# Performance work log

Measured on AMD Instinct MI355X. Metric: run time of the kernel, lower is better.

## Reference

```python
import jax, jax.numpy as jnp
import numpy as np

L, H, C, V, B, T, Q = 6, 8, 512, 32000, 2, 4096, 256
N = C // H
LN_EPS = 1e-5
GN_EPS = 1e-5 * 64  # matches nn.GroupNorm(n_head, C, eps=1e-05*64)


def _shift(x):
    # ZeroPad2d((0,0,1,-1)): x[t] -> x[t-1], zero at t=0
    return jnp.concatenate([jnp.zeros_like(x[:, :1]), x[:, :-1]], axis=1)


def _layernorm(x, w):
    mu = x.mean(-1, keepdims=True)
    var = jnp.var(x, axis=-1, keepdims=True)
    return (x - mu) * jax.lax.rsqrt(var + LN_EPS) * w


def _time_mix(x, maa_k, maa_v, maa_r, maa_g, tdecay, tfaaaa, Wr, Wk, Wv, Wg, Wo, gn_w, gn_b):
    Bsz, Tlen, Cd = x.shape
    xx = _shift(x) - x
    xk = x + xx * maa_k
    xv = x + xx * maa_v
    xr = x + xx * maa_r
    xg = x + xx * maa_g
    r = (xr @ Wr.T).reshape(Bsz, Tlen, H, N).transpose(0, 2, 1, 3)   # B H T N
    k = (xk @ Wk.T).reshape(Bsz, Tlen, H, N).transpose(0, 2, 3, 1)   # B H N T
    v = (xv @ Wv.T).reshape(Bsz, Tlen, H, N).transpose(0, 2, 1, 3)   # B H T N
    g = jax.nn.silu(xg @ Wg.T)
    wdec = jnp.exp(-jnp.exp(tdecay))            # [H], per-head decay in (0,1)
    u = tfaaaa                                  # [H], 'first token' bonus
    ws = (wdec ** Q)[None, :, None, None]       # state decay across a chunk
    jj = jnp.arange(Q)
    wkv = (wdec[:, None] ** (Q - 1 - jj))[None, :, None, :]  # [1,H,1,Q]
    wb = (wdec[:, None] ** jj)[None, :, :, None]              # [1,H,Q,1]
    d = jj[:, None] - jj[None, :]                              # i - j
    # intra-chunk decay matrix: W[i,j] = u (i==j), wdec^(i-j-1) (i>j), 0 (i<j)
    Wmat = jnp.where(d > 0, wdec[:, None, None] ** jnp.maximum(d - 1, 0), 0.0)
    Wmat = (Wmat + u[:, None, None] * jnp.eye(Q, dtype=x.dtype))[None]  # [1,H,Q,Q]
    nc = Tlen // Q
    rc = r.reshape(Bsz, H, nc, Q, N).transpose(2, 0, 1, 3, 4)  # [nc,B,H,Q,N]
    kc = k.reshape(Bsz, H, N, nc, Q).transpose(3, 0, 1, 2, 4)  # [nc,B,H,N,Q]
    vc = v.reshape(Bsz, H, nc, Q, N).transpose(2, 0, 1, 3, 4)  # [nc,B,H,Q,N]

    def step(state, inp):
        rr, kk, vv = inp
        y = ((rr @ kk) * Wmat) @ vv + (rr @ state) * wb
        new_state = ws * state + (kk * wkv) @ vv
        return new_state, y

    state0 = jnp.zeros((Bsz, H, N, N), dtype=x.dtype)
    _, yc = jax.lax.scan(step, state0, (rc, kc, vc))
    y = yc.transpose(1, 2, 0, 3, 4).reshape(Bsz, H, Tlen, N).transpose(0, 2, 1, 3)  # B T H N
    # GroupNorm(n_head groups) == per (b,t,h) normalization over head dim N
    mu = y.mean(-1, keepdims=True)
    var = jnp.var(y, axis=-1, keepdims=True)
    y = (y - mu) * jax.lax.rsqrt(var + GN_EPS)
    y = y.reshape(Bsz, Tlen, Cd) * gn_w + gn_b
    return (y * g) @ Wo.T


def _channel_mix(x, cmaa_k, cmaa_r, Wck, Wcv, Wcr):
    xx = _shift(x) - x
    xk = x + xx * cmaa_k
    xr = x + xx * cmaa_r
    h = jnp.square(jax.nn.relu(xk @ Wck.T))
    h = h @ Wcv.T
    return jax.nn.sigmoid(xr @ Wcr.T) * h


def _forward(idx, wte, wpe, ln1_w, ln2_w, lnf_w, maa_k, maa_v, maa_r, maa_g, tdecay, tfaaaa,
             Wr, Wk, Wv, Wg, Wo, gn_w, gn_b, cmaa_k, cmaa_r, Wck, Wcv, Wcr):
    t = idx.shape[1]
    x = wte[idx] + wpe[:t]
    for l in range(L):
        x = x + _time_mix(_layernorm(x, ln1_w[l]), maa_k[l], maa_v[l], maa_r[l], maa_g[l],
                          tdecay[l], tfaaaa[l], Wr[l], Wk[l], Wv[l], Wg[l], Wo[l], gn_w[l], gn_b[l])
        x = x + _channel_mix(_layernorm(x, ln2_w[l]), cmaa_k[l], cmaa_r[l], Wck[l], Wcv[l], Wcr[l])
    x = _layernorm(x, lnf_w)
    logits = x[:, -1:, :] @ wte.T  # targets=None path: only last position
    return logits


def setup_inputs() -> dict:
    key = jax.random.key(0)
    ks = jax.random.split(key, 12)
    idx = jax.random.randint(ks[0], (B, T), 0, V)
    # structured per-layer init tensors (exact formulas from __init__)
    ddd = np.arange(C, dtype=np.float32) / C
    hh = np.arange(H, dtype=np.float32) / (H - 1)
    maa_k = np.zeros((L, C), np.float32); maa_v = np.zeros((L, C), np.float32)
    maa_r = np.zeros((L, C), np.float32); maa_g = np.zeros((L, C), np.float32)
    tdecay = np.zeros((L, H), np.float32); tfaaaa = np.zeros((L, H), np.float32)
    cmaa_k = np.zeros((L, C), np.float32); cmaa_r = np.zeros((L, C), np.float32)
    for l in range(L):
        r0 = l / max(L - 1, 1)
        r1 = 1.0 - l / L
        maa_k[l] = 1.0 - ddd ** r1
        maa_v[l] = 1.0 - (ddd ** r1 + 0.3 * r0)
        maa_r[l] = 1.0 - ddd ** (0.5 * r1)
        maa_g[l] = 1.0 - ddd ** (0.5 * r1)
        tdecay[l] = -6.0 + 5.0 * hh ** (0.7 + 1.3 * r0)
        tfaaaa[l] = r0 * (1.0 - hh)
        cmaa_k[l] = 1.0 - ddd ** r1
        cmaa_r[l] = 1.0 - ddd ** r1
    s = 0.02
    return {
        'idx': idx,
        'wte': jax.random.normal(ks[1], (V, C), jnp.float32) * s,
        'wpe': jax.random.normal(ks[2], (T, C), jnp.float32) * s,
        'ln1_w': jnp.ones((L, C), jnp.float32),
        'ln2_w': jnp.ones((L, C), jnp.float32),
        'lnf_w': jnp.ones((C,), jnp.float32),
        'maa_k': jnp.asarray(maa_k), 'maa_v': jnp.asarray(maa_v),
        'maa_r': jnp.asarray(maa_r), 'maa_g': jnp.asarray(maa_g),
        'tdecay': jnp.asarray(tdecay), 'tfaaaa': jnp.asarray(tfaaaa),
        'Wr': jax.random.normal(ks[3], (L, C, C), jnp.float32) * s,
        'Wk': jax.random.normal(ks[4], (L, C, C), jnp.float32) * s,
        'Wv': jax.random.normal(ks[5], (L, C, C), jnp.float32) * s,
        'Wg': jax.random.normal(ks[6], (L, C, C), jnp.float32) * s,
        'Wo': jax.random.normal(ks[7], (L, C, C), jnp.float32) * (s / np.sqrt(2 * L)),
        'gn_w': jnp.ones((L, C), jnp.float32),
        'gn_b': jnp.zeros((L, C), jnp.float32),
        'cmaa_k': jnp.asarray(cmaa_k), 'cmaa_r': jnp.asarray(cmaa_r),
        'Wck': jax.random.normal(ks[8], (L, 3 * C, C), jnp.float32) * s,
        'Wcv': jax.random.normal(ks[9], (L, C, 3 * C), jnp.float32) * s,
        'Wcr': jax.random.normal(ks[10], (L, C, C), jnp.float32) * s,
    }


def reference(idx, wte, wpe, ln1_w, ln2_w, lnf_w, maa_k, maa_v, maa_r, maa_g, tdecay, tfaaaa,
              Wr, Wk, Wv, Wg, Wo, gn_w, gn_b, cmaa_k, cmaa_r, Wck, Wcv, Wcr):
    return _forward(idx, wte, wpe, ln1_w, ln2_w, lnf_w, maa_k, maa_v, maa_r, maa_g, tdecay,
                    tfaaaa, Wr, Wk, Wv, Wg, Wo, gn_w, gn_b, cmaa_k, cmaa_r, Wck, Wcv, Wcr)
```

## Files before the change

### kernel.cpp

```cpp
#include <hip/hip_runtime.h>

#define L_ 6
#define H_ 8
#define C_ 512
#define V_ 32000
#define B_ 2
#define T_ 4096
#define Q_ 256
#define N_ 64
#define NC_ 16
#define M_ 8192

typedef unsigned short u16;
typedef __attribute__((ext_vector_type(8))) short bf16x8;
typedef __attribute__((ext_vector_type(4))) float f32x4;

__device__ __forceinline__ float bf2f(u16 u){
  return __uint_as_float(((unsigned int)u) << 16);
}
__device__ __forceinline__ u16 f2bf(float f){
  unsigned int x = __float_as_uint(f);
  return (u16)((x + 0x7fffu + ((x >> 16) & 1u)) >> 16);
}

__device__ __forceinline__ void gl_lds16(const u16* g, u16* l){
  __builtin_amdgcn_global_load_lds((const __attribute__((address_space(1))) void*)g,
                                   (__attribute__((address_space(3))) void*)l, 16, 0, 0);
}

__global__ __launch_bounds__(256) void detect_kernel(const void* __restrict__ probe,
                                                     int* __restrict__ flag){
  __shared__ int cnt;
  if (threadIdx.x == 0) cnt = 0;
  __syncthreads();
  const u16* p = (const u16*)probe;
  int c = 0;
  for (int i = threadIdx.x; i < 2048; i += 256){
    int e = (p[i] >> 7) & 0xFF;
    if (e >= 128) c++;
  }
  atomicAdd(&cnt, c);
  __syncthreads();
  if (threadIdx.x == 0) *flag = (cnt > 32) ? 1 : 0;
}

struct CvtTab { const void* s[23]; int off8[24]; int bstart[24]; };

__global__ __launch_bounds__(256) void convert_all(CvtTab t, u16* __restrict__ pool,
                                                   const int* __restrict__ flag){
  int i = 0;
  #pragma unroll
  for (int k = 1; k < 23; k++) if ((int)blockIdx.x >= t.bstart[k]) i = k;
  const void* sp = t.s[0];
  #pragma unroll
  for (int k = 1; k < 23; k++) if (i == k) sp = t.s[k];
  const int n8 = t.off8[i+1] - t.off8[i];
  const int nb = t.bstart[i+1] - t.bstart[i];
  const int lb = (int)blockIdx.x - t.bstart[i];
  uint4* dp = (uint4*)pool + t.off8[i];
  const int stride = nb * 256;
  int j = lb*256 + (int)threadIdx.x;
  if (*flag){
    const float4* sf = (const float4*)sp;
    for (; j + stride < n8; j += 2*stride){
      float4 a0 = sf[2*j], a1 = sf[2*j+1];
      int j2 = j + stride;
      float4 b0 = sf[2*j2], b1 = sf[2*j2+1];
      uint4 r0, r1;
      r0.x = (unsigned)f2bf(a0.x) | ((unsigned)f2bf(a0.y) << 16);
      r0.y = (unsigned)f2bf(a0.z) | ((unsigned)f2bf(a0.w) << 16);
      r0.z = (unsigned)f2bf(a1.x) | ((unsigned)f2bf(a1.y) << 16);
      r0.w = (unsigned)f2bf(a1.z) | ((unsigned)f2bf(a1.w) << 16);
      r1.x = (unsigned)f2bf(b0.x) | ((unsigned)f2bf(b0.y) << 16);
      r1.y = (unsigned)f2bf(b0.z) | ((unsigned)f2bf(b0.w) << 16);
      r1.z = (unsigned)f2bf(b1.x) | ((unsigned)f2bf(b1.y) << 16);
      r1.w = (unsigned)f2bf(b1.z) | ((unsigned)f2bf(b1.w) << 16);
      dp[j] = r0; dp[j2] = r1;
    }
    for (; j < n8; j += stride){
      float4 a0 = sf[2*j], a1 = sf[2*j+1];
      uint4 r0;
      r0.x = (unsigned)f2bf(a0.x) | ((unsigned)f2bf(a0.y) << 16);
      r0.y = (unsigned)f2bf(a0.z) | ((unsigned)f2bf(a0.w) << 16);
      r0.z = (unsigned)f2bf(a1.x) | ((unsigned)f2bf(a1.y) << 16);
      r0.w = (unsigned)f2bf(a1.z) | ((unsigned)f2bf(a1.w) << 16);
      dp[j] = r0;
    }
  } else {
    const uint4* s4 = (const uint4*)sp;
    for (; j + 3*stride < n8; j += 4*stride){
      uint4 a = s4[j], b = s4[j+stride], c = s4[j+2*stride], d = s4[j+3*stride];
      dp[j] = a; dp[j+stride] = b; dp[j+2*stride] = c; dp[j+3*stride] = d;
    }
    for (; j < n8; j += stride) dp[j] = s4[j];
  }
}

__global__ __launch_bounds__(256) void embed_kernel(const int* __restrict__ idx,
    const u16* __restrict__ wte, const u16* __restrict__ wpe, float* __restrict__ x){
  int row = blockIdx.x;
  int t = row & (T_-1);
  int tok = idx[row];
  const u16* we = wte + (size_t)tok * C_;
  const u16* wp = wpe + (size_t)t * C_;
  float* xo = x + (size_t)row * C_;
  int c = threadIdx.x;
  xo[c]     = bf2f(we[c])     + bf2f(wp[c]);
  xo[c+256] = bf2f(we[c+256]) + bf2f(wp[c+256]);
}

__global__ __launch_bounds__(256) void ln_tmix_kernel(const float* __restrict__ x,
    const u16* __restrict__ w,
    const u16* __restrict__ mk, const u16* __restrict__ mv,
    const u16* __restrict__ mr, const u16* __restrict__ mg,
    u16* __restrict__ xk, u16* __restrict__ xv, u16* __restrict__ xr, u16* __restrict__ xg){
  int row = blockIdx.x; int t = row & (T_-1);
  size_t off = (size_t)row*C_;
  const float* cur = x + off;
  int c = threadIdx.x;
  float v0 = cur[c], v1 = cur[c+256];
  float p0 = 0.f, p1 = 0.f;
  if (t){ p0 = cur[c - C_]; p1 = cur[c+256 - C_]; }
  float s = v0+v1, ss = v0*v0+v1*v1;
  float sp = p0+p1, ssp = p0*p0+p1*p1;
  int lane = c & 63, wid = c >> 6;
  #pragma unroll
  for (int o=32;o>0;o>>=1){
    s  += __shfl_down(s,o,64);  ss  += __shfl_down(ss,o,64);
    sp += __shfl_down(sp,o,64); ssp += __shfl_down(ssp,o,64);
  }
  __shared__ float r1[4], r2[4], r3[4], r4[4];
  if (lane==0){ r1[wid]=s; r2[wid]=ss; r3[wid]=sp; r4[wid]=ssp; }
  __syncthreads();
  if (c==0){
    float a =r1[0]+r1[1]+r1[2]+r1[3], bq=r2[0]+r2[1]+r2[2]+r2[3];
    float ap=r3[0]+r3[1]+r3[2]+r3[3], bp=r4[0]+r4[1]+r4[2]+r4[3];
    float mu  = a *(1.f/C_); float var  = bq*(1.f/C_) - mu*mu;
    float mup = ap*(1.f/C_); float varp = bp*(1.f/C_) - mup*mup;
    r1[0]=mu;  r2[0]=rsqrtf(fmaxf(var ,0.f)+1e-5f);
    r3[0]=mup; r4[0]=rsqrtf(fmaxf(varp,0.f)+1e-5f);
  }
  __syncthreads();
  float mu=r1[0], inv=r2[0], mup=r3[0], invp=r4[0];
  #pragma unroll
  for (int p=0;p<2;p++){
    int cc = c + p*256;
    float wc = bf2f(w[cc]);
    float xc = ((p?v1:v0)-mu)*inv*wc;
    float xp = t ? ((p?p1:p0)-mup)*invp*wc : 0.f;
    float xx = xp - xc;
    xk[off+cc] = f2bf(xc + xx*bf2f(mk[cc]));
    xv[off+cc] = f2bf(xc + xx*bf2f(mv[cc]));
    xr[off+cc] = f2bf(xc + xx*bf2f(mr[cc]));
    xg[off+cc] = f2bf(xc + xx*bf2f(mg[cc]));
  }
}

__global__ __launch_bounds__(256) void ln_cmix_kernel(const float* __restrict__ x,
    const u16* __restrict__ w,
    const u16* __restrict__ mk, const u16* __restrict__ mr,
    u16* __restrict__ xk, u16* __restrict__ xr){
  int row = blockIdx.x; int t = row & (T_-1);
  size_t off = (size_t)row*C_;
  const float* cur = x + off;
  int c = threadIdx.x;
  float v0 = cur[c], v1 = cur[c+256];
  float p0 = 0.f, p1 = 0.f;
  if (t){ p0 = cur[c - C_]; p1 = cur[c+256 - C_]; }
  float s = v0+v1, ss = v0*v0+v1*v1;
  float sp = p0+p1, ssp = p0*p0+p1*p1;
  int lane = c & 63, wid = c >> 6;
  #pragma unroll
  for (int o=32;o>0;o>>=1){
    s  += __shfl_down(s,o,64);  ss  += __shfl_down(ss,o,64);
    sp += __shfl_down(sp,o,64); ssp += __shfl_down(ssp,o,64);
  }
  __shared__ float r1[4], r2[4], r3[4], r4[4];
  if (lane==0){ r1[wid]=s; r2[wid]=ss; r3[wid]=sp; r4[wid]=ssp; }
  __syncthreads();
  if (c==0){
    float a =r1[0]+r1[1]+r1[2]+r1[3], bq=r2[0]+r2[1]+r2[2]+r2[3];
    float ap=r3[0]+r3[1]+r3[2]+r3[3], bp=r4[0]+r4[1]+r4[2]+r4[3];
    float mu  = a *(1.f/C_); float var  = bq*(1.f/C_) - mu*mu;
    float mup = ap*(1.f/C_); float varp = bp*(1.f/C_) - mup*mup;
    r1[0]=mu;  r2[0]=rsqrtf(fmaxf(var ,0.f)+1e-5f);
    r3[0]=mup; r4[0]=rsqrtf(fmaxf(varp,0.f)+1e-5f);
  }
  __syncthreads();
  float mu=r1[0], inv=r2[0], mup=r3[0], invp=r4[0];
  #pragma unroll
  for (int p=0;p<2;p++){
    int cc = c + p*256;
    float wc = bf2f(w[cc]);
    float xc = ((p?v1:v0)-mu)*inv*wc;
    float xp = t ? ((p?p1:p0)-mup)*invp*wc : 0.f;
    float xx = xp - xc;
    xk[off+cc] = f2bf(xc + xx*bf2f(mk[cc]));
    xr[off+cc] = f2bf(xc + xx*bf2f(mr[cc]));
  }
}

__global__ __launch_bounds__(256) void lnf_last(const float* __restrict__ x,
    const u16* __restrict__ w, float* __restrict__ xf){
  int b = blockIdx.x;
  const float* xr = x + ((size_t)b*T_ + (T_-1))*C_;
  int c = threadIdx.x;
  float v0 = xr[c], v1 = xr[c+256];
  float s = v0+v1, ss = v0*v0+v1*v1;
  int lane = c & 63, wid = c >> 6;
  #pragma unroll
  for (int o=32;o>0;o>>=1){ s += __shfl_down(s,o,64); ss += __shfl_down(ss,o,64); }
  __shared__ float r1[4], r2[4];
  if (lane==0){ r1[wid]=s; r2[wid]=ss; }
  __syncthreads();
  if (c==0){
    float a=r1[0]+r1[1]+r1[2]+r1[3], bq=r2[0]+r2[1]+r2[2]+r2[3];
    float mu = a*(1.f/C_);
    float var = bq*(1.f/C_) - mu*mu;
    r1[0]=mu; r2[0]=rsqrtf(fmaxf(var,0.f)+1e-5f);
  }
  __syncthreads();
  float mu=r1[0], inv=r2[0];
  xf[b*C_+c]     = (v0-mu)*inv*bf2f(w[c]);
  xf[b*C_+c+256] = (v1-mu)*inv*bf2f(w[c+256]);
}

#define ACT_F32 0
#define ACT_RELU2_BF16 1
#define ACT_ADD_F32 2
#define ACT_BF16 3
#define ACT_CMIX 4
#define ACT_KT 5
#define ACT_VT 6
#define ACT_SIG_BF16 7

template<int ACT>
__device__ __forceinline__ void gemm_mfma_body(const u16* __restrict__ X, const u16* __restrict__ W,
    float* __restrict__ Yf, u16* __restrict__ Yb, const u16* __restrict__ AuxB,
    u16* __restrict__ Yt, const u16* __restrict__ td,
    int Ndim, int Kdim, int bm, int bn){
  __shared__ __align__(16) u16 SH[128*64 + 64*64];
  u16* Al = SH;
  u16* Bl = SH + 128*64;
  const int tid = threadIdx.x;
  const int wv = tid >> 6, ln = tid & 63;
  const int m16 = ln & 15, q = ln >> 4;

  f32x4 acc[2][4];
  #pragma unroll
  for (int i=0;i<2;i++)
    #pragma unroll
    for (int j=0;j<4;j++) acc[i][j] = f32x4{0.f,0.f,0.f,0.f};

  const int r0 = wv*8 + (ln >> 3);
  const int c0 = (ln & 7)*8;
  const u16* ga = X + (size_t)(bm + r0)*Kdim + c0;
  const u16* gb = W + (size_t)(bn + r0)*Kdim + c0;
  u16* la = Al + r0*64 + c0;
  u16* lb = Bl + r0*64 + c0;

  for (int k0=0; k0<Kdim; k0+=64){
    #pragma unroll
    for (int s=0;s<4;s++)
      gl_lds16(ga + (size_t)(s*32)*Kdim + k0, la + s*2048);
    #pragma unroll
    for (int s=0;s<2;s++)
      gl_lds16(gb + (size_t)(s*32)*Kdim + k0, lb + s*2048);
    __syncthreads();
    #pragma unroll
    for (int kh=0; kh<2; kh++){
      bf16x8 af[2], bfr[4];
      #pragma unroll
      for (int i=0;i<2;i++) af[i]  = *(const bf16x8*)(Al + (wv*32 + i*16 + m16)*64 + kh*32 + q*8);
      #pragma unroll
      for (int j=0;j<4;j++) bfr[j] = *(const bf16x8*)(Bl + (j*16 + m16)*64 + kh*32 + q*8);
      #pragma unroll
      for (int i=0;i<2;i++)
        #pragma unroll
        for (int j=0;j<4;j++)
          acc[i][j] = __builtin_amdgcn_mfma_f32_16x16x32_bf16(af[i], bfr[j], acc[i][j], 0, 0, 0);
    }
    __syncthreads();
  }

  if (ACT==ACT_KT || ACT==ACT_VT){
    u16* TT = SH;
    const float wdec_s = (ACT==ACT_KT) ? expf(-expf(bf2f(td[(bn>>6)&7]))) : 0.f;
    const int tchunk0 = bm & (Q_-1);
    #pragma unroll
    for (int i=0;i<2;i++){
      const int tloc = wv*32 + i*16 + q*4;
      #pragma unroll
      for (int j=0;j<4;j++){
        const int n = j*16 + m16;
        union { ushort4 v; u16 e[4]; } pk;
        #pragma unroll
        for (int r=0;r<4;r++){
          float v = acc[i][j][r];
          if (ACT==ACT_KT){
            Yb[(size_t)(bm + tloc + r)*Ndim + (bn + n)] = f2bf(v);
            pk.e[r] = f2bf(v * powf(wdec_s, (float)(Q_-1 - (tchunk0 + tloc + r))));
          } else {
            pk.e[r] = f2bf(v);
          }
        }
        *(ushort4*)&TT[n*136 + tloc] = pk.v;
      }
    }
    __syncthreads();
    const int bb = bm >> 12, tt0 = bm & (T_-1);
    const int hh = (bn >> 6) & 7;
    const int nn2 = wv*16 + (ln>>2), seg = ln & 3;
    const u16* srcp = TT + nn2*136 + seg*32;
    u16* dstp = Yt + ((size_t)(((bb<<3)+hh)*64 + nn2))*T_ + tt0 + seg*32;
    #pragma unroll
    for (int k2=0;k2<4;k2++)
      *(uint4*)(dstp + k2*8) = *(const uint4*)(srcp + k2*8);
    return;
  }
  #pragma unroll
  for (int i=0;i<2;i++){
    int row = bm + wv*32 + i*16 + q*4;
    #pragma unroll
    for (int j=0;j<4;j++){
      int col = bn + j*16 + m16;
      #pragma unroll
      for (int r=0;r<4;r++){
        size_t off = (size_t)(row + r)*Ndim + col;
        float v = acc[i][j][r];
        if (ACT==ACT_F32) Yf[off] = v;
        else if (ACT==ACT_RELU2_BF16){ float rr = v>0.f ? v : 0.f; Yb[off] = f2bf(rr*rr); }
        else if (ACT==ACT_BF16) Yb[off] = f2bf(v);
        else if (ACT==ACT_SIG_BF16) Yb[off] = f2bf(1.f/(1.f+expf(-v)));
        else if (ACT==ACT_CMIX){ Yf[off] += v * bf2f(AuxB[off]); }
        else Yf[off] += v;
      }
    }
  }
}

template<int ACT>
__global__ __launch_bounds__(256,4) void gemm_mfma(const u16* __restrict__ X, const u16* __restrict__ W,
    float* __restrict__ Yf, u16* __restrict__ Yb, int Ndim, int Kdim){
  gemm_mfma_body<ACT>(X, W, Yf, Yb, nullptr, nullptr, nullptr, Ndim, Kdim,
                      blockIdx.x*128, blockIdx.y*64);
}

__global__ __launch_bounds__(256,4) void gemm4_mfma(const u16* __restrict__ Abase,
    const u16* __restrict__ W0, const u16* __restrict__ W1,
    const u16* __restrict__ W2, const u16* __restrict__ W3,
    u16* __restrict__ Rb, u16* __restrict__ Kb, u16* __restrict__ Kt,
    u16* __restrict__ Vt, u16* __restrict__ Gb, const u16* __restrict__ td){
  const size_t MC = (size_t)M_*C_;
  const int bm = blockIdx.x*128, bn = blockIdx.y*64;
  switch (blockIdx.z){
    case 0:  gemm_mfma_body<ACT_BF16>(Abase + 2*MC, W0, nullptr, Rb, nullptr, nullptr, nullptr,
                                      C_, C_, bm, bn); break;
    case 1:  gemm_mfma_body<ACT_KT>(Abase, W1, nullptr, Kb, nullptr, Kt, td,
                                    C_, C_, bm, bn); break;
    case 2:  gemm_mfma_body<ACT_VT>(Abase + 1*MC, W2, nullptr, nullptr, nullptr, Vt, nullptr,
                                    C_, C_, bm, bn); break;
    default: gemm_mfma_body<ACT_BF16>(Abase + 3*MC, W3, nullptr, Gb, nullptr, nullptr, nullptr,
                                      C_, C_, bm, bn); break;
  }
}

__global__ __launch_bounds__(256,4) void gemm_ck_cr(const u16* __restrict__ MK, const u16* __restrict__ Wck,
    u16* __restrict__ H1, const u16* __restrict__ MV, const u16* __restrict__ Wcr,
    u16* __restrict__ RRb){
  if (blockIdx.y < 24)
    gemm_mfma_body<ACT_RELU2_BF16>(MK, Wck, nullptr, H1, nullptr, nullptr, nullptr, 3*C_, C_,
                                   blockIdx.x*128, blockIdx.y*64);
  else
    gemm_mfma_body<ACT_SIG_BF16>(MV, Wcr, nullptr, RRb, nullptr, nullptr, nullptr, C_, C_,
                                 blockIdx.x*128, (blockIdx.y-24)*64);
}

__global__ __launch_bounds__(256,4) void gemm_cmix(const u16* __restrict__ H1, const u16* __restrict__ Wcv,
    float* __restrict__ X, const u16* __restrict__ RRb){
  gemm_mfma_body<ACT_CMIX>(H1, Wcv, X, nullptr, RRb, nullptr, nullptr, C_, 3*C_,
                           blockIdx.x*128, blockIdx.y*64);
}

__global__ __launch_bounds__(256) void wkv_state_mfma(const u16* __restrict__ Kt,
    const u16* __restrict__ Vt, float* __restrict__ S){
  const int c = blockIdx.x, bh = blockIdx.y;
  const int tid = threadIdx.x, wv = tid >> 6, ln = tid & 63;
  const int m16 = ln & 15, q = ln >> 4;
  const u16* ka = Kt + (size_t)(bh*N_ + wv*16 + m16)*T_ + c*Q_;
  const u16* vb = Vt + (size_t)(bh*N_ + m16)*T_ + c*Q_;
  f32x4 acc[4];
  #pragma unroll
  for (int nt=0;nt<4;++nt) acc[nt] = f32x4{0.f,0.f,0.f,0.f};
  #pragma unroll
  for (int ks=0; ks<8; ++ks){
    bf16x8 af = *(const bf16x8*)(ka + ks*32 + q*8);
    #pragma unroll
    for (int nt=0;nt<4;++nt){
      bf16x8 bv = *(const bf16x8*)(vb + (size_t)(nt*16)*T_ + ks*32 + q*8);
      acc[nt] = __builtin_amdgcn_mfma_f32_16x16x32_bf16(af, bv, acc[nt], 0,0,0);
    }
  }
  float* Sp = S + ((size_t)bh*NC_ + c)*(N_*N_);
  #pragma unroll
  for (int nt=0;nt<4;++nt)
    #pragma unroll
    for (int r=0;r<4;++r)
      Sp[(wv*16 + q*4 + r)*N_ + nt*16 + m16] = acc[nt][r];
}

__global__ __launch_bounds__(256) void wkv_prefix(float* __restrict__ S, const u16* __restrict__ td){
  const int bh = blockIdx.x, h = bh&7;
  const float wdec = expf(-expf(bf2f(td[h])));
  const float wsd = powf(wdec, (float)Q_);
  float* Sp = S + (size_t)bh*NC_*N_*N_;
  for (int e=threadIdx.x; e<N_*N_; e+=256){
    float cur = 0.f;
    for (int cc=0;cc<NC_;++cc){
      float sc = Sp[(size_t)cc*N_*N_ + e];
      Sp[(size_t)cc*N_*N_ + e] = cur;
      cur = wsd*cur + sc;
    }
  }
}

__global__ __launch_bounds__(256) void wkv_fused(const u16* __restrict__ Rb,
    const u16* __restrict__ Kb, const u16* __restrict__ Vt, const float* __restrict__ S,
    const u16* __restrict__ td, const u16* __restrict__ tf,
    const u16* __restrict__ gnw, const u16* __restrict__ gnb, const u16* __restrict__ g,
    u16* __restrict__ out){
  __shared__ float wpow[Q_];
  __shared__ float st[64][68];
  __shared__ float rs[64][68];
  __shared__ __align__(16) float ylds[64][68];
  u16 (*P)[16][72] = reinterpret_cast<u16(*)[16][72]>(&ylds[0][0]);
  const int c = blockIdx.x>>2, ip = blockIdx.x&3;
  const int bh = blockIdx.y, b = bh>>3, h = bh&7;
  const int tid = threadIdx.x, wv = tid >> 6, ln = tid & 63;
  const int m16 = ln & 15, q = ln >> 4;
  const int tx = tid&15, ty = tid>>4;
  const float wdec = expf(-expf(bf2f(td[h])));
  const float uu = bf2f(tf[h]);
  wpow[tid] = powf(wdec, (float)tid);
  const float* Sp = S + ((size_t)bh*NC_ + c)*(N_*N_);
  for (int e=tid;e<N_*N_;e+=256) st[e>>6][e&63] = Sp[e];
  const size_t base = ((size_t)b*T_ + (size_t)c*Q_)*C_ + h*N_;
  const int i0 = ip*64;
  {
    const int rrr = tid >> 6, cc2 = tid & 63;
    for (int it=0;it<16;++it){ int i=it*4+rrr; rs[i][cc2]=bf2f(Rb[base+(size_t)(i0+i)*C_+cc2]); }
  }
  __syncthreads();
  const int iw0 = ip*64 + wv*16;
  const u16* rrow = Rb + base + (size_t)(iw0 + m16)*C_;
  bf16x8 af0 = *(const bf16x8*)(rrow + q*8);
  bf16x8 af1 = *(const bf16x8*)(rrow + 32 + q*8);
  f32x4 acc[4];
  #pragma unroll
  for (int nt=0;nt<4;++nt) acc[nt] = f32x4{0.f,0.f,0.f,0.f};
  const int irow = iw0 + q*4;
  const u16* vtb = Vt + (size_t)(bh*N_)*T_ + (size_t)c*Q_;
  for (int jt=0; jt<=ip; ++jt){
    f32x4 s[4];
    #pragma unroll
    for (int j2=0;j2<4;++j2) s[j2] = f32x4{0.f,0.f,0.f,0.f};
    #pragma unroll
    for (int j2=0;j2<4;++j2){
      const u16* kr = Kb + base + (size_t)(jt*64 + j2*16 + m16)*C_;
      bf16x8 b0 = *(const bf16x8*)(kr + q*8);
      bf16x8 b1 = *(const bf16x8*)(kr + 32 + q*8);
      s[j2] = __builtin_amdgcn_mfma_f32_16x16x32_bf16(af0, b0, s[j2], 0,0,0);
      s[j2] = __builtin_amdgcn_mfma_f32_16x16x32_bf16(af1, b1, s[j2], 0,0,0);
    }
    #pragma unroll
    for (int j2=0;j2<4;++j2){
      int jc = jt*64 + j2*16 + m16;
      #pragma unroll
      for (int r=0;r<4;++r){
        int ic = irow + r;
        float w = (jc < ic) ? wpow[ic-jc-1] : ((jc==ic) ? uu : 0.f);
        P[wv][q*4+r][j2*16+m16] = f2bf(s[j2][r]*w);
      }
    }
    __asm__ volatile("s_waitcnt lgkmcnt(0)" ::: "memory");
    #pragma unroll
    for (int kp=0;kp<2;++kp){
      bf16x8 ap = *(const bf16x8*)&P[wv][m16][kp*32 + q*8];
      #pragma unroll
      for (int nt=0;nt<4;++nt){
        bf16x8 bv = *(const bf16x8*)(vtb + (size_t)(nt*16 + m16)*T_ + jt*64 + kp*32 + q*8);
        acc[nt] = __builtin_amdgcn_mfma_f32_16x16x32_bf16(ap, bv, acc[nt], 0,0,0);
      }
    }
  }
  __syncthreads();
  #pragma unroll
  for (int nt=0;nt<4;++nt)
    #pragma unroll
    for (int r=0;r<4;++r)
      ylds[wv*16 + q*4 + r][nt*16 + m16] = acc[nt][r];
  __syncthreads();
  float acc2[4][4] = {};
  #pragma unroll
  for (int kk4=0;kk4<16;++kk4){
    f32x4 sv[4], rv[4];
    #pragma unroll
    for (int kkk=0;kkk<4;++kkk) sv[kkk] = *(const f32x4*)&st[kk4*4+kkk][tx*4];
    #pragma unroll
    for (int ii=0;ii<4;++ii)    rv[ii]  = *(const f32x4*)&rs[ty*4+ii][kk4*4];
    #pragma unroll
    for (int ii=0;ii<4;++ii)
      #pragma unroll
      for (int kkk=0;kkk<4;++kkk)
        #pragma unroll
        for (int nn=0;nn<4;++nn)
          acc2[ii][nn] += rv[ii][kkk]*sv[kkk][nn];
  }
  #pragma unroll
  for (int ii=0;ii<4;ii++){
    int tl = ty*4+ii;
    int il = i0 + tl;
    size_t roff = base + (size_t)il*C_;
    float w = wpow[il];
    f32x4 yv = *(const f32x4*)&ylds[tl][tx*4];
    float val[4];
    float s=0.f, ss=0.f;
    #pragma unroll
    for (int nn=0;nn<4;nn++){
      float v = yv[nn] + w*acc2[ii][nn];
      val[nn]=v; s+=v; ss+=v*v;
    }
    #pragma unroll
    for (int o=8;o>0;o>>=1){ s+=__shfl_xor(s,o,64); ss+=__shfl_xor(ss,o,64); }
    float mu = s*(1.f/N_);
    float var = ss*(1.f/N_) - mu*mu;
    float inv = rsqrtf(fmaxf(var,0.f) + 6.4e-4f);
    union { ushort4 v; u16 e[4]; } gv, ov;
    gv.v = *(const ushort4*)(g + roff + tx*4);
    #pragma unroll
    for (int nn=0;nn<4;nn++){
      int ci = h*N_ + tx*4 + nn;
      float gg = bf2f(gv.e[nn]);
      float sil = gg/(1.f+expf(-gg));
      ov.e[nn] = f2bf(((val[nn]-mu)*inv*bf2f(gnw[ci]) + bf2f(gnb[ci]))*sil);
    }
    *(ushort4*)(out + roff + tx*4) = ov.v;
  }
}

__global__ __launch_bounds__(256) void logits_kernel(const float* __restrict__ xf,
    const u16* __restrict__ wte, void* __restrict__ out, const int* __restrict__ flag){
  const int wid = threadIdx.x>>6, lane = threadIdx.x&63;
  const int gw = blockIdx.x*4 + wid;
  const int b = gw / V_, v = gw - b*V_;
  const u16* wrow = wte + (size_t)v*C_;
  const float* xr = xf + b*C_;
  union {uint4 q; u16 h[8];} uu;
  uu.q = *(const uint4*)(wrow + lane*8);
  float s = 0.f;
  #pragma unroll
  for (int j=0;j<8;j++) s += bf2f(uu.h[j])*xr[lane*8+j];
  #pragma unroll
  for (int o=32;o>0;o>>=1) s += __shfl_down(s,o,64);
  if (lane==0){
    size_t o = (size_t)b*V_ + v;
    if (*flag) ((float*)out)[o] = s;
    else       ((u16*)out)[o]   = f2bf(s);
  }
}

extern "C" void kernel_launch(void* const* d_in, const int* in_sizes, int n_in,
                              void* d_out, int out_size, void* d_ws, size_t ws_size,
                              hipStream_t stream){
  (void)out_size; (void)ws_size; (void)n_in;
  const int* idx  = (const int*)d_in[0];

  char* ws = (char*)d_ws;
  const size_t MC  = (size_t)M_*C_;
  size_t o = 0;
  int* flag = (int*)(ws + o);            o += 1024;
  float* X   = (float*)(ws + o);         o += MC*4;
  u16* MK = (u16*)(ws + o);              o += MC*2;
  u16* MV = (u16*)(ws + o);              o += MC*2;
  u16* MR = (u16*)(ws + o);              o += MC*2;
  u16* MG = (u16*)(ws + o);              o += MC*2;
  u16* Rb = (u16*)(ws + o);              o += MC*2;
  u16* Kb = (u16*)(ws + o);              o += MC*2;
  u16* Kt = (u16*)(ws + o);              o += MC*2;
  u16* Gb = (u16*)(ws + o);              o += MC*2;
  u16* Vt = (u16*)(ws + o);              o += MC*2;
  float* XF = (float*)(ws + o);          o += 65536;
  u16* pool = (u16*)(ws + o);
  u16* YGN = MK;
  float* S  = (float*)MR;
  u16* H1 = Rb;
  u16* RRb = MR;

  detect_kernel<<<1,256,0,stream>>>(d_in[12], flag);
  u16* cw[24];
  CvtTab tab;
  int nblocks;
  {
    size_t poff = 0; int acc8 = 0, bacc = 0;
    long long total8 = 0;
    for (int i=1;i<24;i++) total8 += (long long)(in_sizes[i] >> 3);
    for (int i=1;i<24;i++){
      cw[i] = pool + poff; poff += (size_t)in_sizes[i];
      tab.s[i-1] = d_in[i];
      tab.off8[i-1] = acc8;
      tab.bstart[i-1] = bacc;
      int n8 = in_sizes[i] >> 3;
      int nb = (int)(((long long)n8 * 2048 + total8 - 1) / total8);
      if (nb < 1) nb = 1;
      acc8 += n8; bacc += nb;
    }
    tab.off8[23] = acc8; tab.bstart[23] = bacc;
    nblocks = bacc;
  }
  convert_all<<<nblocks,256,0,stream>>>(tab, pool, flag);
  const u16* wte  = cw[1];  const u16* wpe  = cw[2];
  const u16* ln1w = cw[3];  const u16* ln2w = cw[4];  const u16* lnfw = cw[5];
  const u16* maak = cw[6];  const u16* maav = cw[7];
  const u16* maar = cw[8];  const u16* maag = cw[9];
  const u16* tdec = cw[10]; const u16* tfir = cw[11];
  const u16* Wr   = cw[12]; const u16* Wk   = cw[13]; const u16* Wv   = cw[14];
  const u16* Wg   = cw[15]; const u16* Wo   = cw[16];
  const u16* gnw  = cw[17]; const u16* gnb  = cw[18];
  const u16* cmk  = cw[19]; const u16* cmr  = cw[20];
  const u16* Wck  = cw[21]; const u16* Wcv  = cw[22]; const u16* Wcr  = cw[23];

  embed_kernel<<<M_,256,0,stream>>>(idx,wte,wpe,X);
  dim3 gsq(M_/128, C_/64);
  dim3 g4 (M_/128, C_/64, 4);
  dim3 gckcr(M_/128, 32);
  for (int l=0;l<L_;++l){
    ln_tmix_kernel<<<M_,256,0,stream>>>(X, ln1w+l*C_, maak+l*C_, maav+l*C_, maar+l*C_,
                                        maag+l*C_, MK,MV,MR,MG);
    gemm4_mfma<<<g4,256,0,stream>>>(MK, Wr+(size_t)l*C_*C_, Wk+(size_t)l*C_*C_,
                                    Wv+(size_t)l*C_*C_, Wg+(size_t)l*C_*C_,
                                    Rb, Kb, Kt, Vt, Gb, tdec+l*H_);
    wkv_state_mfma<<<dim3(NC_, B_*H_),256,0,stream>>>(Kt, Vt, S);
    wkv_prefix<<<B_*H_,256,0,stream>>>(S, tdec+l*H_);
    wkv_fused<<<dim3(NC_*4, B_*H_),256,0,stream>>>(Rb, Kb, Vt, S, tdec+l*H_, tfir+l*H_,
                                                   gnw+l*C_, gnb+l*C_, Gb, YGN);
    gemm_mfma<ACT_ADD_F32><<<gsq,256,0,stream>>>(YGN, Wo+(size_t)l*C_*C_, X, nullptr, C_, C_);
    ln_cmix_kernel<<<M_,256,0,stream>>>(X, ln2w+l*C_, cmk+l*C_, cmr+l*C_, MK, MV);
    gemm_ck_cr<<<gckcr,256,0,stream>>>(MK, Wck+(size_t)l*3*C_*C_, H1,
                                       MV, Wcr+(size_t)l*C_*C_, RRb);
    gemm_cmix<<<gsq,256,0,stream>>>(H1, Wcv+(size_t)l*3*C_*C_, X, RRb);
  }
  lnf_last<<<B_,256,0,stream>>>(X, lnfw, XF);
  logits_kernel<<<(B_*V_)/4,256,0,stream>>>(XF, wte, d_out, flag);
}
```

Before: 1.673 ms.

## Skip bf16 weight copy via pointer table, widen GEMM tiles, split K/V transpose

Adds a device pointer table filled at runtime, so when inputs are already bf16 the kernels read the raw input buffers instead of copying every weight into a pool. The conversion kernel now returns early in that case. The QKVG and channel-mix GEMMs move to 128x128 tiles, and the fused transpose/decay epilogue is pulled out into a separate kvtrans kernel using swizzled LDS. powf is replaced by exp2f. Larger tiles raise register and LDS pressure, and the separate transpose adds an extra pass over K and V.

```diff
diff --git a/kernel.cpp b/kernel.cpp
--- a/kernel.cpp
+++ b/kernel.cpp
@@ -44,10 +44,20 @@
   if (threadIdx.x == 0) *flag = (cnt > 32) ? 1 : 0;
 }
 
+struct PtrTab { const void* raw[23]; long long off[23]; };
+
+__global__ __launch_bounds__(64) void fill_ptab(PtrTab pt, const u16* __restrict__ pool,
+    const int* __restrict__ flag, const u16** __restrict__ ptab){
+  int i = threadIdx.x;
+  if (i < 23)
+    ptab[i+1] = (*flag) ? (pool + pt.off[i]) : (const u16*)pt.raw[i];
+}
+
 struct CvtTab { const void* s[23]; int off8[24]; int bstart[24]; };
 
 __global__ __launch_bounds__(256) void convert_all(CvtTab t, u16* __restrict__ pool,
                                                    const int* __restrict__ flag){
+  if (!*flag) return;
   int i = 0;
   #pragma unroll
   for (int k = 1; k < 23; k++) if ((int)blockIdx.x >= t.bstart[k]) i = k;
@@ -59,45 +69,22 @@
   const int lb = (int)blockIdx.x - t.bstart[i];
   uint4* dp = (uint4*)pool + t.off8[i];
   const int stride = nb * 256;
-  int j = lb*256 + (int)threadIdx.x;
-  if (*flag){
-    const float4* sf = (const float4*)sp;
-    for (; j + stride < n8; j += 2*stride){
-      float4 a0 = sf[2*j], a1 = sf[2*j+1];
-      int j2 = j + stride;
-      float4 b0 = sf[2*j2], b1 = sf[2*j2+1];
-      uint4 r0, r1;
-      r0.x = (unsigned)f2bf(a0.x) | ((unsigned)f2bf(a0.y) << 16);
-      r0.y = (unsigned)f2bf(a0.z) | ((unsigned)f2bf(a0.w) << 16);
-      r0.z = (unsigned)f2bf(a1.x) | ((unsigned)f2bf(a1.y) << 16);
-      r0.w = (unsigned)f2bf(a1.z) | ((unsigned)f2bf(a1.w) << 16);
-      r1.x = (unsigned)f2bf(b0.x) | ((unsigned)f2bf(b0.y) << 16);
-      r1.y = (unsigned)f2bf(b0.z) | ((unsigned)f2bf(b0.w) << 16);
-      r1.z = (unsigned)f2bf(b1.x) | ((unsigned)f2bf(b1.y) << 16);
-      r1.w = (unsigned)f2bf(b1.z) | ((unsigned)f2bf(b1.w) << 16);
-      dp[j] = r0; dp[j2] = r1;
-    }
-    for (; j < n8; j += stride){
-      float4 a0 = sf[2*j], a1 = sf[2*j+1];
-      uint4 r0;
-      r0.x = (unsigned)f2bf(a0.x) | ((unsigned)f2bf(a0.y) << 16);
-      r0.y = (unsigned)f2bf(a0.z) | ((unsigned)f2bf(a0.w) << 16);
-      r0.z = (unsigned)f2bf(a1.x) | ((unsigned)f2bf(a1.y) << 16);
-      r0.w = (unsigned)f2bf(a1.z) | ((unsigned)f2bf(a1.w) << 16);
-      dp[j] = r0;
-    }
-  } else {
-    const uint4* s4 = (const uint4*)sp;
-    for (; j + 3*stride < n8; j += 4*stride){
-      uint4 a = s4[j], b = s4[j+stride], c = s4[j+2*stride], d = s4[j+3*stride];
-      dp[j] = a; dp[j+stride] = b; dp[j+2*stride] = c; dp[j+3*stride] = d;
-    }
-    for (; j < n8; j += stride) dp[j] = s4[j];
+  const float4* sf = (const float4*)sp;
+  for (int j = lb*256 + (int)threadIdx.x; j < n8; j += stride){
+    float4 a0 = sf[2*j], a1 = sf[2*j+1];
+    uint4 r0;
+    r0.x = (unsigned)f2bf(a0.x) | ((unsigned)f2bf(a0.y) << 16);
+    r0.y = (unsigned)f2bf(a0.z) | ((unsigned)f2bf(a0.w) << 16);
+    r0.z = (unsigned)f2bf(a1.x) | ((unsigned)f2bf(a1.y) << 16);
+    r0.w = (unsigned)f2bf(a1.z) | ((unsigned)f2bf(a1.w) << 16);
+    dp[j] = r0;
   }
 }
 
 __global__ __launch_bounds__(256) void embed_kernel(const int* __restrict__ idx,
-    const u16* __restrict__ wte, const u16* __restrict__ wpe, float* __restrict__ x){
+    const u16* const* __restrict__ ptab, float* __restrict__ x){
+  const u16* wte = ptab[1];
+  const u16* wpe = ptab[2];
   int row = blockIdx.x;
   int t = row & (T_-1);
   int tok = idx[row];
@@ -110,10 +97,13 @@
 }
 
 __global__ __launch_bounds__(256) void ln_tmix_kernel(const float* __restrict__ x,
-    const u16* __restrict__ w,
-    const u16* __restrict__ mk, const u16* __restrict__ mv,
-    const u16* __restrict__ mr, const u16* __restrict__ mg,
+    const u16* const* __restrict__ ptab, int l,
     u16* __restrict__ xk, u16* __restrict__ xv, u16* __restrict__ xr, u16* __restrict__ xg){
+  const u16* w  = ptab[3] + l*C_;
+  const u16* mk = ptab[6] + l*C_;
+  const u16* mv = ptab[7] + l*C_;
+  const u16* mr = ptab[8] + l*C_;
+  const u16* mg = ptab[9] + l*C_;
   int row = blockIdx.x; int t = row & (T_-1);
   size_t off = (size_t)row*C_;
   const float* cur = x + off;
@@ -157,9 +147,11 @@
 }
 
 __global__ __launch_bounds__(256) void ln_cmix_kernel(const float* __restrict__ x,
-    const u16* __restrict__ w,
-    const u16* __restrict__ mk, const u16* __restrict__ mr,
+    const u16* const* __restrict__ ptab, int l,
     u16* __restrict__ xk, u16* __restrict__ xr){
+  const u16* w  = ptab[4]  + l*C_;
+  const u16* mk = ptab[19] + l*C_;
+  const u16* mr = ptab[20] + l*C_;
   int row = blockIdx.x; int t = row & (T_-1);
   size_t off = (size_t)row*C_;
   const float* cur = x + off;
@@ -201,7 +193,8 @@
 }
 
 __global__ __launch_bounds__(256) void lnf_last(const float* __restrict__ x,
-    const u16* __restrict__ w, float* __restrict__ xf){
+    const u16* const* __restrict__ ptab, float* __restrict__ xf){
+  const u16* w = ptab[5];
   int b = blockIdx.x;
   const float* xr = x + ((size_t)b*T_ + (T_-1))*C_;
   int c = threadIdx.x;
@@ -225,23 +218,18 @@
   xf[b*C_+c+256] = (v1-mu)*inv*bf2f(w[c+256]);
 }
 
-#define ACT_F32 0
 #define ACT_RELU2_BF16 1
 #define ACT_ADD_F32 2
 #define ACT_BF16 3
 #define ACT_CMIX 4
-#define ACT_KT 5
-#define ACT_VT 6
 #define ACT_SIG_BF16 7
 
 template<int ACT>
 __device__ __forceinline__ void gemm_mfma_body(const u16* __restrict__ X, const u16* __restrict__ W,
     float* __restrict__ Yf, u16* __restrict__ Yb, const u16* __restrict__ AuxB,
-    u16* __restrict__ Yt, const u16* __restrict__ td,
     int Ndim, int Kdim, int bm, int bn){
-  __shared__ __align__(16) u16 SH[128*64 + 64*64];
-  u16* Al = SH;
-  u16* Bl = SH + 128*64;
+  __shared__ __align__(16) u16 Al[128*64];
+  __shared__ __align__(16) u16 Bl[64*64];
   const int tid = threadIdx.x;
   const int wv = tid >> 6, ln = tid & 63;
   const int m16 = ln & 15, q = ln >> 4;
@@ -283,41 +271,6 @@
     __syncthreads();
   }
 
-  if (ACT==ACT_KT || ACT==ACT_VT){
-    u16* TT = SH;
-    const float wdec_s = (ACT==ACT_KT) ? expf(-expf(bf2f(td[(bn>>6)&7]))) : 0.f;
-    const int tchunk0 = bm & (Q_-1);
-    #pragma unroll
-    for (int i=0;i<2;i++){
-      const int tloc = wv*32 + i*16 + q*4;
-      #pragma unroll
-      for (int j=0;j<4;j++){
-        const int n = j*16 + m16;
-        union { ushort4 v; u16 e[4]; } pk;
-        #pragma unroll
-        for (int r=0;r<4;r++){
-          float v = acc[i][j][r];
-          if (ACT==ACT_KT){
-            Yb[(size_t)(bm + tloc + r)*Ndim + (bn + n)] = f2bf(v);
-            pk.e[r] = f2bf(v * powf(wdec_s, (float)(Q_-1 - (tchunk0 + tloc + r))));
-          } else {
-            pk.e[r] = f2bf(v);
-          }
-        }
-        *(ushort4*)&TT[n*136 + tloc] = pk.v;
-      }
-    }
-    __syncthreads();
-    const int bb = bm >> 12, tt0 = bm & (T_-1);
-    const int hh = (bn >> 6) & 7;
-    const int nn2 = wv*16 + (ln>>2), seg = ln & 3;
-    const u16* srcp = TT + nn2*136 + seg*32;
-    u16* dstp = Yt + ((size_t)(((bb<<3)+hh)*64 + nn2))*T_ + tt0 + seg*32;
-    #pragma unroll
-    for (int k2=0;k2<4;k2++)
-      *(uint4*)(dstp + k2*8) = *(const uint4*)(srcp + k2*8);
-    return;
-  }
   #pragma unroll
   for (int i=0;i<2;i++){
     int row = bm + wv*32 + i*16 + q*4;
@@ -328,58 +281,153 @@
       for (int r=0;r<4;r++){
         size_t off = (size_t)(row + r)*Ndim + col;
         float v = acc[i][j][r];
-        if (ACT==ACT_F32) Yf[off] = v;
+        if (ACT==ACT_ADD_F32) Yf[off] += v;
+        else if (ACT==ACT_CMIX){ Yf[off] += v * bf2f(AuxB[off]); }
+        else if (ACT==ACT_BF16) Yb[off] = f2bf(v);
+      }
+    }
+  }
+}
+
+template<int ACT>
+__device__ __forceinline__ void gemm128_body(const u16* __restrict__ X, const u16* __restrict__ W,
+    u16* __restrict__ Yb, int Ndim, int Kdim, int bm, int bn){
+  __shared__ __align__(16) u16 Al[128*64];
+  __shared__ __align__(16) u16 Bl[128*64];
+  const int tid = threadIdx.x;
+  const int wv = tid >> 6, ln = tid & 63;
+  const int m16 = ln & 15, q = ln >> 4;
+
+  f32x4 acc[2][8];
+  #pragma unroll
+  for (int i=0;i<2;i++)
+    #pragma unroll
+    for (int j=0;j<8;j++) acc[i][j] = f32x4{0.f,0.f,0.f,0.f};
+
+  const int r0 = wv*8 + (ln >> 3);
+  const int c0 = (ln & 7)*8;
+  const u16* ga = X + (size_t)(bm + r0)*Kdim + c0;
+  const u16* gb = W + (size_t)(bn + r0)*Kdim + c0;
+  u16* la = Al + r0*64 + c0;
+  u16* lb = Bl + r0*64 + c0;
+
+  for (int k0=0; k0<Kdim; k0+=64){
+    #pragma unroll
+    for (int s=0;s<4;s++)
+      gl_lds16(ga + (size_t)(s*32)*Kdim + k0, la + s*2048);
+    #pragma unroll
+    for (int s=0;s<4;s++)
+      gl_lds16(gb + (size_t)(s*32)*Kdim + k0, lb + s*2048);
+    __syncthreads();
+    #pragma unroll
+    for (int kh=0; kh<2; kh++){
+      bf16x8 af0 = *(const bf16x8*)(Al + (wv*32 + m16)*64      + kh*32 + q*8);
+      bf16x8 af1 = *(const bf16x8*)(Al + (wv*32 + 16 + m16)*64 + kh*32 + q*8);
+      #pragma unroll
+      for (int j=0;j<8;j++){
+        bf16x8 bfr = *(const bf16x8*)(Bl + (j*16 + m16)*64 + kh*32 + q*8);
+        acc[0][j] = __builtin_amdgcn_mfma_f32_16x16x32_bf16(af0, bfr, acc[0][j], 0, 0, 0);
+        acc[1][j] = __builtin_amdgcn_mfma_f32_16x16x32_bf16(af1, bfr, acc[1][j], 0, 0, 0);
+      }
+    }
+    __syncthreads();
+  }
+
+  #pragma unroll
+  for (int i=0;i<2;i++){
+    int row = bm + wv*32 + i*16 + q*4;
+    #pragma unroll
+    for (int j=0;j<8;j++){
+      int col = bn + j*16 + m16;
+      #pragma unroll
+      for (int r=0;r<4;r++){
+        size_t off = (size_t)(row + r)*Ndim + col;
+        float v = acc[i][j][r];
+        if (ACT==ACT_BF16) Yb[off] = f2bf(v);
         else if (ACT==ACT_RELU2_BF16){ float rr = v>0.f ? v : 0.f; Yb[off] = f2bf(rr*rr); }
-        else if (ACT==ACT_BF16) Yb[off] = f2bf(v);
         else if (ACT==ACT_SIG_BF16) Yb[off] = f2bf(1.f/(1.f+expf(-v)));
-        else if (ACT==ACT_CMIX){ Yf[off] += v * bf2f(AuxB[off]); }
-        else Yf[off] += v;
       }
     }
   }
 }
 
-template<int ACT>
-__global__ __launch_bounds__(256,4) void gemm_mfma(const u16* __restrict__ X, const u16* __restrict__ W,
-    float* __restrict__ Yf, u16* __restrict__ Yb, int Ndim, int Kdim){
-  gemm_mfma_body<ACT>(X, W, Yf, Yb, nullptr, nullptr, nullptr, Ndim, Kdim,
-                      blockIdx.x*128, blockIdx.y*64);
-}
-
-__global__ __launch_bounds__(256,4) void gemm4_mfma(const u16* __restrict__ Abase,
-    const u16* __restrict__ W0, const u16* __restrict__ W1,
-    const u16* __restrict__ W2, const u16* __restrict__ W3,
-    u16* __restrict__ Rb, u16* __restrict__ Kb, u16* __restrict__ Kt,
-    u16* __restrict__ Vt, u16* __restrict__ Gb, const u16* __restrict__ td){
+__global__ __launch_bounds__(256,3) void gemm4_mfma(const u16* const* __restrict__ ptab, int l,
+    const u16* __restrict__ Abase,
+    u16* __restrict__ Rb, u16* __restrict__ Kb, u16* __restrict__ Vb, u16* __restrict__ Gb){
   const size_t MC = (size_t)M_*C_;
-  const int bm = blockIdx.x*128, bn = blockIdx.y*64;
+  const size_t ws = (size_t)l*C_*C_;
+  const int bm = blockIdx.x*128, bn = blockIdx.y*128;
   switch (blockIdx.z){
-    case 0:  gemm_mfma_body<ACT_BF16>(Abase + 2*MC, W0, nullptr, Rb, nullptr, nullptr, nullptr,
-                                      C_, C_, bm, bn); break;
-    case 1:  gemm_mfma_body<ACT_KT>(Abase, W1, nullptr, Kb, nullptr, Kt, td,
-                                    C_, C_, bm, bn); break;
-    case 2:  gemm_mfma_body<ACT_VT>(Abase + 1*MC, W2, nullptr, nullptr, nullptr, Vt, nullptr,
-                                    C_, C_, bm, bn); break;
-    default: gemm_mfma_body<ACT_BF16>(Abase + 3*MC, W3, nullptr, Gb, nullptr, nullptr, nullptr,
-                                      C_, C_, bm, bn); break;
-  }
-}
-
-__global__ __launch_bounds__(256,4) void gemm_ck_cr(const u16* __restrict__ MK, const u16* __restrict__ Wck,
-    u16* __restrict__ H1, const u16* __restrict__ MV, const u16* __restrict__ Wcr,
-    u16* __restrict__ RRb){
-  if (blockIdx.y < 24)
-    gemm_mfma_body<ACT_RELU2_BF16>(MK, Wck, nullptr, H1, nullptr, nullptr, nullptr, 3*C_, C_,
-                                   blockIdx.x*128, blockIdx.y*64);
+    case 0:  gemm128_body<ACT_BF16>(Abase + 2*MC, ptab[12]+ws, Rb, C_, C_, bm, bn); break;
+    case 1:  gemm128_body<ACT_BF16>(Abase,        ptab[13]+ws, Kb, C_, C_, bm, bn); break;
+    case 2:  gemm128_body<ACT_BF16>(Abase + 1*MC, ptab[14]+ws, Vb, C_, C_, bm, bn); break;
+    default: gemm128_body<ACT_BF16>(Abase + 3*MC, ptab[15]+ws, Gb, C_, C_, bm, bn); break;
+  }
+}
+
+__global__ __launch_bounds__(256,3) void gemm_ck_cr(const u16* const* __restrict__ ptab, int l,
+    const u16* __restrict__ MK, u16* __restrict__ H1,
+    const u16* __restrict__ MV, u16* __restrict__ RRb){
+  if (blockIdx.y < 12)
+    gemm128_body<ACT_RELU2_BF16>(MK, ptab[21]+(size_t)l*3*C_*C_, H1, 3*C_, C_,
+                                 blockIdx.x*128, blockIdx.y*128);
   else
-    gemm_mfma_body<ACT_SIG_BF16>(MV, Wcr, nullptr, RRb, nullptr, nullptr, nullptr, C_, C_,
-                                 blockIdx.x*128, (blockIdx.y-24)*64);
-}
-
-__global__ __launch_bounds__(256,4) void gemm_cmix(const u16* __restrict__ H1, const u16* __restrict__ Wcv,
-    float* __restrict__ X, const u16* __restrict__ RRb){
-  gemm_mfma_body<ACT_CMIX>(H1, Wcv, X, nullptr, RRb, nullptr, nullptr, C_, 3*C_,
-                           blockIdx.x*128, blockIdx.y*64);
+    gemm128_body<ACT_SIG_BF16>(MV, ptab[23]+(size_t)l*C_*C_, RRb, C_, C_,
+                               blockIdx.x*128, (blockIdx.y-12)*128);
+}
+
+__global__ __launch_bounds__(256,4) void gemm_wo(const u16* const* __restrict__ ptab, int l,
+    const u16* __restrict__ YGN, float* __restrict__ X){
+  gemm_mfma_body<ACT_ADD_F32>(YGN, ptab[16]+(size_t)l*C_*C_, X, nullptr, nullptr,
+                              C_, C_, blockIdx.x*128, blockIdx.y*64);
+}
+
+__global__ __launch_bounds__(256,4) void gemm_cmix(const u16* const* __restrict__ ptab, int l,
+    const u16* __restrict__ H1, float* __restrict__ X, const u16* __restrict__ RRb){
+  gemm_mfma_body<ACT_CMIX>(H1, ptab[22]+(size_t)l*3*C_*C_, X, nullptr, RRb,
+                           C_, 3*C_, blockIdx.x*128, blockIdx.y*64);
+}
+
+__global__ __launch_bounds__(256) void kvtrans(const u16* __restrict__ Kb, const u16* __restrict__ Vb,
+    u16* __restrict__ Kt, u16* __restrict__ Vt, const u16* const* __restrict__ ptab, int l){
+  __shared__ __align__(16) u16 tile[64*64];
+  const int t0 = blockIdx.x*64, bh = blockIdx.y, b = bh>>3, h = bh&7;
+  const bool isK = (blockIdx.z == 1);
+  const u16* src = isK ? Kb : Vb;
+  u16* dst = isK ? Kt : Vt;
+  float l2w = 0.f;
+  if (isK){
+    const u16* td = ptab[10] + l*H_;
+    l2w = -expf(bf2f(td[h])) * 1.44269504f;
+  }
+  const int tid = threadIdx.x;
+  #pragma unroll
+  for (int it=0; it<2; ++it){
+    int tl = it*32 + (tid>>3);
+    int n0 = (tid&7)*8;
+    union {uint4 q; u16 e[8];} v;
+    v.q = *(const uint4*)(src + ((size_t)(b*T_ + t0 + tl))*C_ + h*N_ + n0);
+    if (isK){
+      int tloc = (t0 + tl) & (Q_-1);
+      float sc = exp2f(l2w * (float)(Q_-1 - tloc));
+      #pragma unroll
+      for (int e=0;e<8;++e) v.e[e] = f2bf(bf2f(v.e[e])*sc);
+    }
+    int col = n0 ^ (((tl>>3)&7)<<3);
+    *(uint4*)&tile[tl*64 + col] = v.q;
+  }
+  __syncthreads();
+  #pragma unroll
+  for (int it=0; it<2; ++it){
+    int nl = it*32 + (tid>>3);
+    int t0l = (tid&7)*8;
+    int swz = (tid&7)<<3;
+    union {uint4 q; u16 h2[8];} pk;
+    #pragma unroll
+    for (int e=0;e<8;++e)
+      pk.h2[e] = tile[(t0l+e)*64 + (nl ^ swz)];
+    *(uint4*)(dst + ((size_t)(bh*N_ + nl))*T_ + t0 + t0l) = pk.q;
+  }
 }
 
 __global__ __launch_bounds__(256) void wkv_state_mfma(const u16* __restrict__ Kt,
@@ -409,10 +457,12 @@
       Sp[(wv*16 + q*4 + r)*N_ + nt*16 + m16] = acc[nt][r];
 }
 
-__global__ __launch_bounds__(256) void wkv_prefix(float* __restrict__ S, const u16* __restrict__ td){
+__global__ __launch_bounds__(256) void wkv_prefix(float* __restrict__ S,
+    const u16* const* __restrict__ ptab, int l){
   const int bh = blockIdx.x, h = bh&7;
-  const float wdec = expf(-expf(bf2f(td[h])));
-  const float wsd = powf(wdec, (float)Q_);
+  const u16* td = ptab[10] + l*H_;
+  const float l2w = -expf(bf2f(td[h])) * 1.44269504f;
+  const float wsd = exp2f(l2w * (float)Q_);
   float* Sp = S + (size_t)bh*NC_*N_*N_;
   for (int e=threadIdx.x; e<N_*N_; e+=256){
     float cur = 0.f;
@@ -426,22 +476,25 @@
 
 __global__ __launch_bounds__(256) void wkv_fused(const u16* __restrict__ Rb,
     const u16* __restrict__ Kb, const u16* __restrict__ Vt, const float* __restrict__ S,
-    const u16* __restrict__ td, const u16* __restrict__ tf,
-    const u16* __restrict__ gnw, const u16* __restrict__ gnb, const u16* __restrict__ g,
-    u16* __restrict__ out){
+    const u16* const* __restrict__ ptab, int l,
+    const u16* __restrict__ g, u16* __restrict__ out){
   __shared__ float wpow[Q_];
   __shared__ float st[64][68];
   __shared__ float rs[64][68];
   __shared__ __align__(16) float ylds[64][68];
   u16 (*P)[16][72] = reinterpret_cast<u16(*)[16][72]>(&ylds[0][0]);
+  const u16* td  = ptab[10] + l*H_;
+  const u16* tf  = ptab[11] + l*H_;
+  const u16* gnw = ptab[17] + l*C_;
+  const u16* gnb = ptab[18] + l*C_;
   const int c = blockIdx.x>>2, ip = blockIdx.x&3;
   const int bh = blockIdx.y, b = bh>>3, h = bh&7;
   const int tid = threadIdx.x, wv = tid >> 6, ln = tid & 63;
   const int m16 = ln & 15, q = ln >> 4;
   const int tx = tid&15, ty = tid>>4;
-  const float wdec = expf(-expf(bf2f(td[h])));
+  const float l2w = -expf(bf2f(td[h])) * 1.44269504f;
   const float uu = bf2f(tf[h]);
-  wpow[tid] = powf(wdec, (float)tid);
+  wpow[tid] = exp2f(l2w * (float)tid);
   const float* Sp = S + ((size_t)bh*NC_ + c)*(N_*N_);
   for (int e=tid;e<N_*N_;e+=256) st[e>>6][e&63] = Sp[e];
   const size_t base = ((size_t)b*T_ + (size_t)c*Q_)*C_ + h*N_;
@@ -549,7 +602,8 @@
 }
 
 __global__ __launch_bounds__(256) void logits_kernel(const float* __restrict__ xf,
-    const u16* __restrict__ wte, void* __restrict__ out, const int* __restrict__ flag){
+    const u16* const* __restrict__ ptab, void* __restrict__ out, const int* __restrict__ flag){
+  const u16* wte = ptab[1];
   const int wid = threadIdx.x>>6, lane = threadIdx.x&63;
   const int gw = blockIdx.x*4 + wid;
   const int b = gw / V_, v = gw - b*V_;
@@ -579,6 +633,7 @@
   const size_t MC  = (size_t)M_*C_;
   size_t o = 0;
   int* flag = (int*)(ws + o);            o += 1024;
+  const u16** ptab = (const u16**)(ws + o); o += 1024;
   float* X   = (float*)(ws + o);         o += MC*4;
   u16* MK = (u16*)(ws + o);              o += MC*2;
   u16* MV = (u16*)(ws + o);              o += MC*2;
@@ -586,8 +641,9 @@
   u16* MG = (u16*)(ws + o);              o += MC*2;
   u16* Rb = (u16*)(ws + o);              o += MC*2;
   u16* Kb = (u16*)(ws + o);              o += MC*2;
+  u16* Vb = (u16*)(ws + o);              o += MC*2;
+  u16* Gb = (u16*)(ws + o);              o += MC*2;
   u16* Kt = (u16*)(ws + o);              o += MC*2;
-  u16* Gb = (u16*)(ws + o);              o += MC*2;
   u16* Vt = (u16*)(ws + o);              o += MC*2;
   float* XF = (float*)(ws + o);          o += 65536;
   u16* pool = (u16*)(ws + o);
@@ -597,15 +653,16 @@
   u16* RRb = MR;
 
   detect_kernel<<<1,256,0,stream>>>(d_in[12], flag);
-  u16* cw[24];
-  CvtTab tab;
+  CvtTab tab; PtrTab pt;
   int nblocks;
   {
     size_t poff = 0; int acc8 = 0, bacc = 0;
     long long total8 = 0;
     for (int i=1;i<24;i++) total8 += (long long)(in_sizes[i] >> 3);
     for (int i=1;i<24;i++){
-      cw[i] = pool + poff; poff += (size_t)in_sizes[i];
+      pt.raw[i-1] = d_in[i];
+      pt.off[i-1] = (long long)poff;
+      poff += (size_t)in_sizes[i];
       tab.s[i-1] = d_in[i];
       tab.off8[i-1] = acc8;
       tab.bstart[i-1] = bacc;
@@ -617,38 +674,26 @@
     tab.off8[23] = acc8; tab.bstart[23] = bacc;
     nblocks = bacc;
   }
+  fill_ptab<<<1,64,0,stream>>>(pt, pool, flag, ptab);
   convert_all<<<nblocks,256,0,stream>>>(tab, pool, flag);
-  const u16* wte  = cw[1];  const u16* wpe  = cw[2];
-  const u16* ln1w = cw[3];  const u16* ln2w = cw[4];  const u16* lnfw = cw[5];
-  const u16* maak = cw[6];  const u16* maav = cw[7];
-  const u16* maar = cw[8];  const u16* maag = cw[9];
-  const u16* tdec = cw[10]; const u16* tfir = cw[11];
-  const u16* Wr   = cw[12]; const u16* Wk   = cw[13]; const u16* Wv   = cw[14];
-  const u16* Wg   = cw[15]; const u16* Wo   = cw[16];
-  const u16* gnw  = cw[17]; const u16* gnb  = cw[18];
-  const u16* cmk  = cw[19]; const u16* cmr  = cw[20];
-  const u16* Wck  = cw[21]; const u16* Wcv  = cw[22]; const u16* Wcr  = cw[23];
-
-  embed_kernel<<<M_,256,0,stream>>>(idx,wte,wpe,X);
-  dim3 gsq(M_/128, C_/64);
-  dim3 g4 (M_/128, C_/64, 4);
-  dim3 gckcr(M_/128, 32);
+
+  embed_kernel<<<M_,256,0,stream>>>(idx, ptab, X);
+  dim3 g4 (M_/128, C_/128, 4);
+  dim3 gkv(T_/64, B_*H_, 2);
+  dim3 gck(M_/128, 16);
+  dim3 gwo(M_/128, C_/64);
   for (int l=0;l<L_;++l){
-    ln_tmix_kernel<<<M_,256,0,stream>>>(X, ln1w+l*C_, maak+l*C_, maav+l*C_, maar+l*C_,
-                                        maag+l*C_, MK,MV,MR,MG);
-    gemm4_mfma<<<g4,256,0,stream>>>(MK, Wr+(size_t)l*C_*C_, Wk+(size_t)l*C_*C_,
-                                    Wv+(size_t)l*C_*C_, Wg+(size_t)l*C_*C_,
-                                    Rb, Kb, Kt, Vt, Gb, tdec+l*H_);
+    ln_tmix_kernel<<<M_,256,0,stream>>>(X, ptab, l, MK,MV,MR,MG);
+    gemm4_mfma<<<g4,256,0,stream>>>(ptab, l, MK, Rb, Kb, Vb, Gb);
+    kvtrans<<<gkv,256,0,stream>>>(Kb, Vb, Kt, Vt, ptab, l);
     wkv_state_mfma<<<dim3(NC_, B_*H_),256,0,stream>>>(Kt, Vt, S);
-    wkv_prefix<<<B_*H_,256,0,stream>>>(S, tdec+l*H_);
-    wkv_fused<<<dim3(NC_*4, B_*H_),256,0,stream>>>(Rb, Kb, Vt, S, tdec+l*H_, tfir+l*H_,
-                                                   gnw+l*C_, gnb+l*C_, Gb, YGN);
-    gemm_mfma<ACT_ADD_F32><<<gsq,256,0,stream>>>(YGN, Wo+(size_t)l*C_*C_, X, nullptr, C_, C_);
-    ln_cmix_kernel<<<M_,256,0,stream>>>(X, ln2w+l*C_, cmk+l*C_, cmr+l*C_, MK, MV);
-    gemm_ck_cr<<<gckcr,256,0,stream>>>(MK, Wck+(size_t)l*3*C_*C_, H1,
-                                       MV, Wcr+(size_t)l*C_*C_, RRb);
-    gemm_cmix<<<gsq,256,0,stream>>>(H1, Wcv+(size_t)l*3*C_*C_, X, RRb);
-  }
-  lnf_last<<<B_,256,0,stream>>>(X, lnfw, XF);
-  logits_kernel<<<(B_*V_)/4,256,0,stream>>>(XF, wte, d_out, flag);
-}
+    wkv_prefix<<<B_*H_,256,0,stream>>>(S, ptab, l);
+    wkv_fused<<<dim3(NC_*4, B_*H_),256,0,stream>>>(Rb, Kb, Vt, S, ptab, l, Gb, YGN);
+    gemm_wo<<<gwo,256,0,stream>>>(ptab, l, YGN, X);
+    ln_cmix_kernel<<<M_,256,0,stream>>>(X, ptab, l, MK, MV);
+    gemm_ck_cr<<<gck,256,0,stream>>>(ptab, l, MK, H1, MV, RRb);
+    gemm_cmix<<<gwo,256,0,stream>>>(ptab, l, H1, X, RRb);
+  }
+  lnf_last<<<B_,256,0,stream>>>(X, ptab, XF);
+  logits_kernel<<<(B_*V_)/4,256,0,stream>>>(XF, ptab, d_out, flag);
+}
```

Result: slower. 1.711 ms (+2.3%).
